# Optimization experiments

Measured on AMD Instinct MI355X. Metric: run time of the kernel, lower is better.

Reference implementation:

```python
import jax, jax.numpy as jnp
import numpy as np
import math

N_HEAD = 16
N_LATENTS = 64
CHUNK = 128
ROPE_THETA = 10000.0


def _rope_cos_sin(T, D, theta):
    # D = head_dim; freqs over D/2 pairs
    inv = 1.0 / (theta ** (jnp.arange(0, D, 2, dtype=jnp.float32) / D))  # [D/2]
    ang = jnp.arange(T, dtype=jnp.float32)[:, None] * inv[None, :]       # [T, D/2]
    return jnp.cos(ang), jnp.sin(ang)


def _apply_rope(k, cos, sin):
    # k: [B, T, H, D]; pairs are consecutive (2i, 2i+1)
    B, T, H, D = k.shape
    kr = k.reshape(B, T, H, D // 2, 2)
    a, b = kr[..., 0], kr[..., 1]
    c = cos[None, :, None, :]
    s = sin[None, :, None, :]
    out = jnp.stack([a * c - b * s, a * s + b * c], axis=-1)
    return out.reshape(B, T, H, D).astype(k.dtype)


def setup_inputs() -> dict:
    key = jax.random.key(0)
    ks = jax.random.split(key, 6)
    B, T, C = 8, 4096, 1024
    H, L = N_HEAD, N_LATENTS
    D = C // H
    std_in = 1.0 / math.sqrt(C)
    return {
        "x": jax.random.normal(ks[0], (B, T, C), jnp.float32),
        "latent_queries": jax.random.normal(ks[1], (1, L, H, D), jnp.float32) * (1.0 / math.sqrt(D)),
        "W_k": jax.random.normal(ks[2], (C, C), jnp.float32) * std_in,
        "W_v": jax.random.normal(ks[3], (C, C), jnp.float32) * std_in,
        "W_g": jax.random.normal(ks[4], (H * L, C), jnp.float32) * std_in,
        "W_p": jax.random.normal(ks[5], (C, C), jnp.float32) * std_in,
    }


def reference(x, latent_queries, W_k, W_v, W_g, W_p):
    B, T, C = x.shape
    H, L, cs = N_HEAD, N_LATENTS, CHUNK
    D = C // H
    scale = 1.0 / math.sqrt(D)

    k = (x @ W_k.T).reshape(B, T, H, D)
    v = (x @ W_v.T).reshape(B, T, H, D)
    cos, sin = _rope_cos_sin(T, D, ROPE_THETA)
    k = _apply_rope(k, cos, sin)

    # softmax-gated latent mixing weights: [B, T, H, L]
    gates = jax.nn.softmax((x @ W_g.T).reshape(B, T, H, L) * scale, axis=-1)

    q = jnp.transpose(latent_queries, (0, 2, 1, 3))          # [1, H, L, D]
    nc = T // cs
    kc = jnp.transpose(k, (0, 2, 1, 3)).reshape(B, H, nc, cs, D)
    vc = jnp.transpose(v, (0, 2, 1, 3)).reshape(B, H, nc, cs, D)

    # per-chunk SDPA with torch is_causal semantics: top-left aligned
    # lower-triangular mask (latent row i attends chunk cols j <= i)
    scores = jnp.einsum('zhld,bhncd->bhnlc', q, kc) * scale   # [B,H,nc,L,cs]
    causal = jnp.arange(cs)[None, :] <= jnp.arange(L)[:, None]  # [L, cs]
    scores = jnp.where(causal[None, None, None], scores, -jnp.inf)
    probs = jax.nn.softmax(scores, axis=-1)
    # matmul with V per chunk, SUM over chunks (as in the torch loop)
    attn = jnp.einsum('bhnlc,bhncd->bhld', probs, vc)         # [B,H,L,D]

    # weighted combine: einsum('bhls,bhtl->bhts') then [B,T,C]
    weighted = jnp.einsum('bhld,bthl->bthd', attn, gates)
    out = weighted.reshape(B, T, C) @ W_p.T
    return out
```

## Files before the change

### kernel.cpp

```cpp
#include <hip/hip_runtime.h>
#include <hip/hip_bf16.h>

typedef unsigned short u16;
typedef __attribute__((ext_vector_type(8))) short bf16x8;
typedef __attribute__((ext_vector_type(4))) float f32x4;
typedef __attribute__((ext_vector_type(4))) unsigned short u16x4;

#define DEVI static __device__ __forceinline__

DEVI u16 f2bf(float f) {
    union { __hip_bfloat16 h; u16 u; } cv;
    cv.h = __float2bfloat16(f);
    return cv.u;
}
DEVI float bf2f(u16 u) {
    union { u16 u; __hip_bfloat16 h; } cv;
    cv.u = u;
    return __bfloat162float(cv.h);
}

DEVI void gload_lds16(const void* g, void* l) {
    __builtin_amdgcn_global_load_lds(
        (const __attribute__((address_space(1))) unsigned int*)g,
        (__attribute__((address_space(3))) unsigned int*)l, 16, 0, 0);
}

__global__ void k_cvt(const float* __restrict__ in, u16* __restrict__ out, int n4) {
    int i = blockIdx.x * blockDim.x + threadIdx.x;
    int stride = gridDim.x * blockDim.x;
    for (; i < n4; i += stride) {
        float4 v = ((const float4*)in)[i];
        u16x4 o;
        o.x = f2bf(v.x); o.y = f2bf(v.y); o.z = f2bf(v.z); o.w = f2bf(v.w);
        ((u16x4*)out)[i] = o;
    }
}

__global__ void k_rope(float2* __restrict__ tab) {
    int i = blockIdx.x * 256 + threadIdx.x;
    int t = i >> 5, j = i & 31;
    float inv = powf(10000.f, -(float)j / 32.f);
    float ang = (float)t * inv;
    float s, c;
    sincosf(ang, &s, &c);
    tab[i] = make_float2(c, s);
}

template<int MODE>
__global__ __launch_bounds__(256, 2) void k_gemm(
    const u16* __restrict__ A, const u16* __restrict__ Bw,
    void* __restrict__ Cout, const float2* __restrict__ rope)
{
    constexpr int K = 1024;
    __shared__ u16 As[128 * 32];
    __shared__ u16 Bs[128 * 32];
    const int tid = threadIdx.x;
    const int lane = tid & 63, wid = tid >> 6;
    const int wr = wid >> 1, wc = wid & 1;
    const int row0 = blockIdx.y * 128, col0 = blockIdx.x * 128;

    int r0 = row0 + (tid >> 2);
    int r1 = r0 + 64;
    if (MODE == 0) {
        r0 = ((r0 >> 11) << 12) | (((r0 >> 6) & 31) << 7) | (r0 & 63);
        r1 = ((r1 >> 11) << 12) | (((r1 >> 6) & 31) << 7) | (r1 & 63);
    }
    const int kcol = (tid & 3) * 8;
    const u16* gA0 = A + (size_t)r0 * K + kcol;
    const u16* gA1 = A + (size_t)r1 * K + kcol;
    const u16* gB0 = Bw + (size_t)(col0 + (tid >> 2)) * K + kcol;
    const u16* gB1 = gB0 + (size_t)64 * K;

    char* AsB = (char*)As + wid * 1024;
    char* BsB = (char*)Bs + wid * 1024;

    f32x4 acc[4][4];
#pragma unroll
    for (int i = 0; i < 4; ++i)
#pragma unroll
        for (int j = 0; j < 4; ++j) acc[i][j] = f32x4{0.f, 0.f, 0.f, 0.f};

#pragma unroll 1
    for (int kt = 0; kt < K / 32; ++kt) {
        gload_lds16(gA0, AsB);
        gload_lds16(gA1, AsB + 4096);
        gload_lds16(gB0, BsB);
        gload_lds16(gB1, BsB + 4096);
        gA0 += 32; gA1 += 32; gB0 += 32; gB1 += 32;
        __syncthreads();
        const int koff = (lane >> 4) * 8;
        bf16x8 af[4], bfr[4];
#pragma unroll
        for (int mf = 0; mf < 4; ++mf)
            af[mf] = *(const bf16x8*)&As[(wr * 64 + mf * 16 + (lane & 15)) * 32 + koff];
#pragma unroll
        for (int nf = 0; nf < 4; ++nf)
            bfr[nf] = *(const bf16x8*)&Bs[(wc * 64 + nf * 16 + (lane & 15)) * 32 + koff];
#pragma unroll
        for (int mf = 0; mf < 4; ++mf)
#pragma unroll
            for (int nf = 0; nf < 4; ++nf)
                acc[mf][nf] = __builtin_amdgcn_mfma_f32_16x16x32_bf16(af[mf], bfr[nf], acc[mf][nf], 0, 0, 0);
        __syncthreads();
    }

    const int rbase = row0 + wr * 64 + (lane >> 4) * 4;
    const int cbase = col0 + wc * 64 + (lane & 15);
#pragma unroll
    for (int mf = 0; mf < 4; ++mf) {
#pragma unroll
        for (int nf = 0; nf < 4; ++nf) {
            const int gc = cbase + nf * 16;
#pragma unroll
            for (int r = 0; r < 4; ++r) {
                const int gr = rbase + mf * 16 + r;
                float v = acc[mf][nf][r];
                if (MODE == 0) {
                    float o = __shfl_xor(v, 1);
                    float res;
                    if (gc < 1024) {
                        int t = (((gr >> 6) & 31) << 7) | (gr & 63);
                        float2 cs = rope[t * 32 + ((gc & 63) >> 1)];
                        res = (gc & 1) ? (o * cs.y + v * cs.x) : (v * cs.x - o * cs.y);
                    } else {
                        res = v;
                    }
                    ((u16*)Cout)[(size_t)gr * 2048 + gc] = f2bf(res);
                } else if (MODE == 1) {
                    ((u16*)Cout)[(size_t)gr * 1024 + gc] = f2bf(v);
                } else {
                    ((float*)Cout)[(size_t)gr * 1024 + gc] = v;
                }
            }
        }
    }
}

__global__ __launch_bounds__(256, 2) void k_attn(
    const u16* __restrict__ kv, const float* __restrict__ lq, float* __restrict__ attnT)
{
    __shared__ char smem[65536];
    const int tid = threadIdx.x;
    const int lane = tid & 63, wid = tid >> 6;
    const int gidx = blockIdx.x & 3;
    const int bh = blockIdx.x >> 2;
    const int b = bh >> 4, h = bh & 15;

    bf16x8 qf[4][2];
#pragma unroll
    for (int lb = 0; lb < 4; ++lb)
#pragma unroll
        for (int kb = 0; kb < 2; ++kb) {
            const float* src = lq + ((size_t)(lb * 16 + (lane & 15)) * 16 + h) * 64 + kb * 32 + (lane >> 4) * 8;
            float4 v0 = ((const float4*)src)[0];
            float4 v1 = ((const float4*)src)[1];
            union { bf16x8 v; u16 u[8]; } pk;
            pk.u[0] = f2bf(v0.x * 0.125f); pk.u[1] = f2bf(v0.y * 0.125f);
            pk.u[2] = f2bf(v0.z * 0.125f); pk.u[3] = f2bf(v0.w * 0.125f);
            pk.u[4] = f2bf(v1.x * 0.125f); pk.u[5] = f2bf(v1.y * 0.125f);
            pk.u[6] = f2bf(v1.z * 0.125f); pk.u[7] = f2bf(v1.w * 0.125f);
            qf[lb][kb] = pk.v;
        }

    char* Pl = smem + wid * 16384;
    char* Vb = smem + wid * 16384 + 8192;
    u16* Vl = (u16*)Vb;

    f32x4 accT[4][4];
#pragma unroll
    for (int i = 0; i < 4; ++i)
#pragma unroll
        for (int j = 0; j < 4; ++j) accT[i][j] = f32x4{0.f, 0.f, 0.f, 0.f};

#pragma unroll 1
    for (int ci = 0; ci < 2; ++ci) {
        const int n = gidx * 8 + wid * 2 + ci;
        const size_t krow = (size_t)b * 2048 + (size_t)n * 64;

#pragma unroll
        for (int j = 0; j < 8; ++j) {
            const u16* g = kv + (krow + j * 8 + (lane >> 3)) * 2048 + 1024 + h * 64 + (lane & 7) * 8;
            gload_lds16(g, Vb + j * 1024);
        }

        f32x4 S[4][4];
#pragma unroll
        for (int i = 0; i < 4; ++i)
#pragma unroll
            for (int j = 0; j < 4; ++j) S[i][j] = f32x4{0.f, 0.f, 0.f, 0.f};
#pragma unroll
        for (int kb = 0; kb < 2; ++kb) {
            bf16x8 kf[4];
#pragma unroll
            for (int cb = 0; cb < 4; ++cb)
                kf[cb] = *(const bf16x8*)(kv + (krow + cb * 16 + (lane & 15)) * 2048 + h * 64 + kb * 32 + (lane >> 4) * 8);
#pragma unroll
            for (int lb = 0; lb < 4; ++lb)
#pragma unroll
                for (int cb = 0; cb < 4; ++cb)
                    S[lb][cb] = __builtin_amdgcn_mfma_f32_16x16x32_bf16(qf[lb][kb], kf[cb], S[lb][cb], 0, 0, 0);
        }

#pragma unroll
        for (int lb = 0; lb < 4; ++lb) {
#pragma unroll
            for (int r = 0; r < 4; ++r) {
                const int l = lb * 16 + (lane >> 4) * 4 + r;
                const int c0 = lane & 15;
                float vv[4];
                float m = -3e30f;
#pragma unroll
                for (int cb = 0; cb < 4; ++cb) {
                    int c = cb * 16 + c0;
                    vv[cb] = (c <= l) ? S[lb][cb][r] : -3e30f;
                    m = fmaxf(m, vv[cb]);
                }
                m = fmaxf(m, __shfl_xor(m, 1));
                m = fmaxf(m, __shfl_xor(m, 2));
                m = fmaxf(m, __shfl_xor(m, 4));
                m = fmaxf(m, __shfl_xor(m, 8));
                float p[4];
                float sum = 0.f;
#pragma unroll
                for (int cb = 0; cb < 4; ++cb) {
                    int c = cb * 16 + c0;
                    p[cb] = (c <= l) ? __expf(vv[cb] - m) : 0.f;
                    sum += p[cb];
                }
                sum += __shfl_xor(sum, 1);
                sum += __shfl_xor(sum, 2);
                sum += __shfl_xor(sum, 4);
                sum += __shfl_xor(sum, 8);
                const float inv = 1.f / sum;
#pragma unroll
                for (int cb = 0; cb < 4; ++cb) {
                    int c = cb * 16 + c0;
                    int byte = (l * 128 + c * 2) ^ ((l & 7) << 4);
                    *(u16*)(Pl + byte) = f2bf(p[cb] * inv);
                }
            }
        }

        asm volatile("s_waitcnt vmcnt(0)" ::: "memory");

#pragma unroll
        for (int kb = 0; kb < 2; ++kb) {
            bf16x8 pf[4];
#pragma unroll
            for (int lf = 0; lf < 4; ++lf) {
                int l = lf * 16 + (lane & 15);
                int byte = (l * 128 + (kb * 32 + (lane >> 4) * 8) * 2) ^ ((l & 7) << 4);
                pf[lf] = *(const bf16x8*)(Pl + byte);
            }
#pragma unroll
            for (int mf = 0; mf < 4; ++mf) {
                const int d = mf * 16 + (lane & 15);
                const int cb2 = kb * 32 + (lane >> 4) * 8;
                union { bf16x8 v; u16 u[8]; } vt;
#pragma unroll
                for (int e = 0; e < 8; ++e) vt.u[e] = Vl[(cb2 + e) * 64 + d];
#pragma unroll
                for (int lf = 0; lf < 4; ++lf)
                    accT[mf][lf] = __builtin_amdgcn_mfma_f32_16x16x32_bf16(vt.v, pf[lf], accT[mf][lf], 0, 0, 0);
            }
        }
    }

    float* red = (float*)smem;
#pragma unroll
    for (int mf = 0; mf < 4; ++mf)
#pragma unroll
        for (int lf = 0; lf < 4; ++lf)
#pragma unroll
            for (int r = 0; r < 4; ++r)
                red[wid * 4096 + (mf * 16 + (lane >> 4) * 4 + r) * 64 + lf * 16 + (lane & 15)] = accT[mf][lf][r];
    __syncthreads();
    for (int idx = tid; idx < 4096; idx += 256) {
        float s = red[idx] + red[4096 + idx] + red[8192 + idx] + red[12288 + idx];
        atomicAdd(&attnT[(size_t)bh * 4096 + idx], s);
    }
}

__global__ __launch_bounds__(256, 4) void k_weighted(
    const u16* __restrict__ logits, const float* __restrict__ attnT, u16* __restrict__ wout)
{
    const int tid = threadIdx.x, lane = tid & 63, wid = tid >> 6;
    const int bh = blockIdx.x >> 5, tt = blockIdx.x & 31;
    const int b = bh >> 4, h = bh & 15;
    const int t0 = tt * 128 + wid * 32;

    const float* at = attnT + (size_t)bh * 4096;
    bf16x8 bfr[4][2];
#pragma unroll
    for (int nf = 0; nf < 4; ++nf)
#pragma unroll
        for (int kb = 0; kb < 2; ++kb) {
            const float* src = at + (nf * 16 + (lane & 15)) * 64 + kb * 32 + (lane >> 4) * 8;
            float4 v0 = ((const float4*)src)[0];
            float4 v1 = ((const float4*)src)[1];
            union { bf16x8 v; u16 u[8]; } pk;
            pk.u[0] = f2bf(v0.x); pk.u[1] = f2bf(v0.y); pk.u[2] = f2bf(v0.z); pk.u[3] = f2bf(v0.w);
            pk.u[4] = f2bf(v1.x); pk.u[5] = f2bf(v1.y); pk.u[6] = f2bf(v1.z); pk.u[7] = f2bf(v1.w);
            bfr[nf][kb] = pk.v;
        }

    f32x4 acc[2][4];
#pragma unroll
    for (int i = 0; i < 2; ++i)
#pragma unroll
        for (int j = 0; j < 4; ++j) acc[i][j] = f32x4{0.f, 0.f, 0.f, 0.f};

#pragma unroll
    for (int mf = 0; mf < 2; ++mf) {
        const int t = t0 + mf * 16 + (lane & 15);
        const u16* lrow = logits + ((size_t)b * 4096 + t) * 1024 + h * 64 + (lane >> 4) * 8;
        bf16x8 l0 = *(const bf16x8*)lrow;
        bf16x8 l1 = *(const bf16x8*)(lrow + 32);
        float va[16];
#pragma unroll
        for (int j = 0; j < 8; ++j) {
            va[j] = bf2f((u16)l0[j]) * 0.125f;
            va[8 + j] = bf2f((u16)l1[j]) * 0.125f;
        }
        float m = va[0];
#pragma unroll
        for (int j = 1; j < 16; ++j) m = fmaxf(m, va[j]);
        m = fmaxf(m, __shfl_xor(m, 16));
        m = fmaxf(m, __shfl_xor(m, 32));
        float sum = 0.f;
#pragma unroll
        for (int j = 0; j < 16; ++j) { va[j] = __expf(va[j] - m); sum += va[j]; }
        sum += __shfl_xor(sum, 16);
        sum += __shfl_xor(sum, 32);
        const float inv = 1.f / sum;
        union { bf16x8 v; u16 u[8]; } a0, a1;
#pragma unroll
        for (int j = 0; j < 8; ++j) {
            a0.u[j] = f2bf(va[j] * inv);
            a1.u[j] = f2bf(va[8 + j] * inv);
        }
#pragma unroll
        for (int nf = 0; nf < 4; ++nf) {
            acc[mf][nf] = __builtin_amdgcn_mfma_f32_16x16x32_bf16(a0.v, bfr[nf][0], acc[mf][nf], 0, 0, 0);
            acc[mf][nf] = __builtin_amdgcn_mfma_f32_16x16x32_bf16(a1.v, bfr[nf][1], acc[mf][nf], 0, 0, 0);
        }
    }

#pragma unroll
    for (int mf = 0; mf < 2; ++mf)
#pragma unroll
        for (int nf = 0; nf < 4; ++nf)
#pragma unroll
            for (int r = 0; r < 4; ++r) {
                int t = t0 + mf * 16 + (lane >> 4) * 4 + r;
                wout[((size_t)b * 4096 + t) * 1024 + h * 64 + nf * 16 + (lane & 15)] = f2bf(acc[mf][nf][r]);
            }
}

extern "C" void kernel_launch(void* const* d_in, const int* in_sizes, int n_in,
                              void* d_out, int out_size, void* d_ws, size_t ws_size,
                              hipStream_t stream)
{
    const float* x  = (const float*)d_in[0];
    const float* lq = (const float*)d_in[1];
    const float* Wk = (const float*)d_in[2];
    const float* Wv = (const float*)d_in[3];
    const float* Wg = (const float*)d_in[4];
    const float* Wp = (const float*)d_in[5];

    char* ws = (char*)d_ws;
    u16*    wkv   = (u16*)(ws + 0);
    u16*    wg    = (u16*)(ws + 4194304);
    u16*    wp    = (u16*)(ws + 6291456);
    float2* rope  = (float2*)(ws + 8388608);
    float*  attnT = (float*)(ws + 9437184);
    u16*    kv    = (u16*)(ws + 11534336);
    u16* logits = (u16*)d_out;
    u16* xb     = (u16*)((char*)d_out + 67108864);

    hipMemsetAsync(attnT, 0, 128 * 4096 * sizeof(float), stream);

    k_cvt<<<2048, 256, 0, stream>>>(x, xb, 33554432 / 4);
    k_cvt<<<512, 256, 0, stream>>>(Wk, wkv, 1048576 / 4);
    k_cvt<<<512, 256, 0, stream>>>(Wv, wkv + 1048576, 1048576 / 4);
    k_cvt<<<512, 256, 0, stream>>>(Wg, wg, 1048576 / 4);
    k_cvt<<<512, 256, 0, stream>>>(Wp, wp, 1048576 / 4);
    k_rope<<<512, 256, 0, stream>>>(rope);

    k_gemm<0><<<dim3(16, 128), 256, 0, stream>>>(xb, wkv, kv, rope);
    k_gemm<1><<<dim3(8, 256), 256, 0, stream>>>(xb, wg, logits, nullptr);
    k_attn<<<512, 256, 0, stream>>>(kv, lq, attnT);
    k_weighted<<<4096, 256, 0, stream>>>(logits, attnT, kv);
    k_gemm<2><<<dim3(8, 256), 256, 0, stream>>>(kv, wp, d_out, nullptr);
}
```

Measured before the change: 613.5 us.

## Replace 128x128 GEMM with pipelined 256x256 tile kernel and XCD-aware block mapping

Rewrites the bf16 GEMM used for the K/V, gate and output projections as a 512-thread, 256x256-tile kernel with a 64-wide K step. It double-buffers 128 KB of dynamic LDS and issues global-to-LDS loads several stages ahead, using explicit vmcnt waits and barriers. It also raises MFMA priority with s_setprio and remaps block indices so neighbouring tiles land on the same XCD. The aim is to hide memory latency and raise operand reuse per LDS load. In exchange it uses far more LDS and registers per block, and the hand-placed waitcnt and barrier schedule is fragile.

```diff
diff --git a/kernel.cpp b/kernel.cpp
--- a/kernel.cpp
+++ b/kernel.cpp
@@ -24,6 +24,9 @@
         (const __attribute__((address_space(1))) unsigned int*)g,
         (__attribute__((address_space(3))) unsigned int*)l, 16, 0, 0);
 }
+
+#define BAR asm volatile("s_barrier" ::: "memory")
+#define VMW(N) asm volatile("s_waitcnt vmcnt(" #N ")" ::: "memory")
 
 __global__ void k_cvt(const float* __restrict__ in, u16* __restrict__ out, int n4) {
     int i = blockIdx.x * blockDim.x + threadIdx.x;
@@ -47,67 +50,116 @@
 }
 
 template<int MODE>
-__global__ __launch_bounds__(256, 2) void k_gemm(
+__global__ __launch_bounds__(512, 2) void k_gemm256(
     const u16* __restrict__ A, const u16* __restrict__ Bw,
     void* __restrict__ Cout, const float2* __restrict__ rope)
 {
-    constexpr int K = 1024;
-    __shared__ u16 As[128 * 32];
-    __shared__ u16 Bs[128 * 32];
+    extern __shared__ char lds[];
     const int tid = threadIdx.x;
     const int lane = tid & 63, wid = tid >> 6;
-    const int wr = wid >> 1, wc = wid & 1;
-    const int row0 = blockIdx.y * 128, col0 = blockIdx.x * 128;
-
-    int r0 = row0 + (tid >> 2);
-    int r1 = r0 + 64;
-    if (MODE == 0) {
-        r0 = ((r0 >> 11) << 12) | (((r0 >> 6) & 31) << 7) | (r0 & 63);
-        r1 = ((r1 >> 11) << 12) | (((r1 >> 6) & 31) << 7) | (r1 & 63);
-    }
-    const int kcol = (tid & 3) * 8;
-    const u16* gA0 = A + (size_t)r0 * K + kcol;
-    const u16* gA1 = A + (size_t)r1 * K + kcol;
-    const u16* gB0 = Bw + (size_t)(col0 + (tid >> 2)) * K + kcol;
-    const u16* gB1 = gB0 + (size_t)64 * K;
-
-    char* AsB = (char*)As + wid * 1024;
-    char* BsB = (char*)Bs + wid * 1024;
-
-    f32x4 acc[4][4];
-#pragma unroll
-    for (int i = 0; i < 4; ++i)
-#pragma unroll
-        for (int j = 0; j < 4; ++j) acc[i][j] = f32x4{0.f, 0.f, 0.f, 0.f};
+    const int wr = wid >> 2, wc = wid & 3;
+    const int koff = (lane >> 4) * 16;
+
+    const int GX = (MODE == 0) ? 8 : 4;
+    const int kx = GX >> 1;
+    int orig = blockIdx.x + blockIdx.y * GX;
+    int xcd = orig & 7, i = orig >> 3;
+    int bx = (xcd % kx) * 2 + (i & 1);
+    int by = (xcd / kx) * 32 + (i >> 1);
+    const int row0 = by * 256, col0 = bx * 256;
+
+    auto stage = [&](int s) {
+        const int t = s >> 2;
+        const int isB = s & 1;
+        const int kh = (s >> 1) & 1;
+        char* base = lds + isB * 65536 + (t & 1) * 32768 + kh * 16384;
+        const int kbase = t * 64 + kh * 32;
+#pragma unroll
+        for (int j = 0; j < 2; ++j) {
+            int idx = j * 512 + tid;
+            int r = idx >> 2;
+            int kc = idx & 3;
+            int grow;
+            if (isB) {
+                grow = col0 + r;
+            } else {
+                grow = row0 + r;
+                if (MODE == 0)
+                    grow = ((grow >> 11) << 12) | (((grow >> 6) & 31) << 7) | (grow & 63);
+            }
+            const u16* g = (isB ? Bw : A) + (size_t)grow * 1024 + kbase + kc * 8;
+            gload_lds16(g, base + j * 8192 + wid * 1024);
+        }
+    };
+
+    bf16x8 af[8];
+    bf16x8 bq[2];
+    f32x4 acc[8][4];
+#pragma unroll
+    for (int m = 0; m < 8; ++m)
+#pragma unroll
+        for (int n = 0; n < 4; ++n) acc[m][n] = f32x4{0.f, 0.f, 0.f, 0.f};
+
+#define LDA(T, KH) do { \
+    const char* ab_ = lds + ((T) & 1) * 32768 + (KH) * 16384; \
+    _Pragma("unroll") \
+    for (int mf = 0; mf < 8; ++mf) \
+        af[mf] = *(const bf16x8*)(ab_ + (wr * 128 + mf * 16 + (lane & 15)) * 64 + koff); \
+} while (0)
+
+#define LDB(T, KH, NH) do { \
+    const char* bb_ = lds + 65536 + ((T) & 1) * 32768 + (KH) * 16384; \
+    bq[0] = *(const bf16x8*)(bb_ + (wc * 64 + ((NH) * 2)     * 16 + (lane & 15)) * 64 + koff); \
+    bq[1] = *(const bf16x8*)(bb_ + (wc * 64 + ((NH) * 2 + 1) * 16 + (lane & 15)) * 64 + koff); \
+} while (0)
+
+#define MMA(NH) do { \
+    __builtin_amdgcn_s_setprio(1); \
+    _Pragma("unroll") \
+    for (int mf = 0; mf < 8; ++mf) { \
+        acc[mf][2 * (NH)]     = __builtin_amdgcn_mfma_f32_16x16x32_bf16(af[mf], bq[0], acc[mf][2 * (NH)], 0, 0, 0); \
+        acc[mf][2 * (NH) + 1] = __builtin_amdgcn_mfma_f32_16x16x32_bf16(af[mf], bq[1], acc[mf][2 * (NH) + 1], 0, 0, 0); \
+    } \
+    __builtin_amdgcn_s_setprio(0); \
+} while (0)
 
 #pragma unroll 1
-    for (int kt = 0; kt < K / 32; ++kt) {
-        gload_lds16(gA0, AsB);
-        gload_lds16(gA1, AsB + 4096);
-        gload_lds16(gB0, BsB);
-        gload_lds16(gB1, BsB + 4096);
-        gA0 += 32; gA1 += 32; gB0 += 32; gB1 += 32;
-        __syncthreads();
-        const int koff = (lane >> 4) * 8;
-        bf16x8 af[4], bfr[4];
-#pragma unroll
-        for (int mf = 0; mf < 4; ++mf)
-            af[mf] = *(const bf16x8*)&As[(wr * 64 + mf * 16 + (lane & 15)) * 32 + koff];
-#pragma unroll
-        for (int nf = 0; nf < 4; ++nf)
-            bfr[nf] = *(const bf16x8*)&Bs[(wc * 64 + nf * 16 + (lane & 15)) * 32 + koff];
-#pragma unroll
-        for (int mf = 0; mf < 4; ++mf)
-#pragma unroll
-            for (int nf = 0; nf < 4; ++nf)
-                acc[mf][nf] = __builtin_amdgcn_mfma_f32_16x16x32_bf16(af[mf], bfr[nf], acc[mf][nf], 0, 0, 0);
-        __syncthreads();
-    }
-
-    const int rbase = row0 + wr * 64 + (lane >> 4) * 4;
+    for (int s = 0; s < 7; ++s) stage(s);
+    VMW(10);
+    BAR;
+
+#pragma unroll 1
+    for (int t = 0; t < 14; ++t) {
+        LDA(t, 0); LDB(t, 0, 0);
+        stage(4 * t + 7);
+        BAR; MMA(0); BAR;
+        LDB(t, 0, 1);
+        stage(4 * t + 8);
+        BAR; MMA(1); VMW(10); BAR;
+        LDA(t, 1); LDB(t, 1, 0);
+        stage(4 * t + 9);
+        BAR; MMA(0); BAR;
+        LDB(t, 1, 1);
+        stage(4 * t + 10);
+        BAR; MMA(1); VMW(10); BAR;
+    }
+    LDA(14, 0); LDB(14, 0, 0); stage(63); BAR; MMA(0); BAR;
+    LDB(14, 0, 1);                         BAR; MMA(1); VMW(8); BAR;
+    LDA(14, 1); LDB(14, 1, 0);             BAR; MMA(0); BAR;
+    LDB(14, 1, 1);                         BAR; MMA(1); VMW(4); BAR;
+    LDA(15, 0); LDB(15, 0, 0);             BAR; MMA(0); BAR;
+    LDB(15, 0, 1);                         BAR; MMA(1); VMW(0); BAR;
+    LDA(15, 1); LDB(15, 1, 0);             BAR; MMA(0); BAR;
+    LDB(15, 1, 1);                         BAR; MMA(1);
+
+#undef LDA
+#undef LDB
+#undef MMA
+
+    const int rbase = row0 + wr * 128 + ((lane >> 4) << 2);
     const int cbase = col0 + wc * 64 + (lane & 15);
 #pragma unroll
-    for (int mf = 0; mf < 4; ++mf) {
+    for (int mf = 0; mf < 8; ++mf) {
 #pragma unroll
         for (int nf = 0; nf < 4; ++nf) {
             const int gc = cbase + nf * 16;
@@ -378,6 +430,10 @@
     u16* logits = (u16*)d_out;
     u16* xb     = (u16*)((char*)d_out + 67108864);
 
+    hipFuncSetAttribute((const void*)k_gemm256<0>, hipFuncAttributeMaxDynamicSharedMemorySize, 131072);
+    hipFuncSetAttribute((const void*)k_gemm256<1>, hipFuncAttributeMaxDynamicSharedMemorySize, 131072);
+    hipFuncSetAttribute((const void*)k_gemm256<2>, hipFuncAttributeMaxDynamicSharedMemorySize, 131072);
+
     hipMemsetAsync(attnT, 0, 128 * 4096 * sizeof(float), stream);
 
     k_cvt<<<2048, 256, 0, stream>>>(x, xb, 33554432 / 4);
@@ -387,9 +443,9 @@
     k_cvt<<<512, 256, 0, stream>>>(Wp, wp, 1048576 / 4);
     k_rope<<<512, 256, 0, stream>>>(rope);
 
-    k_gemm<0><<<dim3(16, 128), 256, 0, stream>>>(xb, wkv, kv, rope);
-    k_gemm<1><<<dim3(8, 256), 256, 0, stream>>>(xb, wg, logits, nullptr);
+    k_gemm256<0><<<dim3(8, 64), 512, 131072, stream>>>(xb, wkv, kv, rope);
+    k_gemm256<1><<<dim3(4, 128), 512, 131072, stream>>>(xb, wg, logits, nullptr);
     k_attn<<<512, 256, 0, stream>>>(kv, lq, attnT);
     k_weighted<<<4096, 256, 0, stream>>>(logits, attnT, kv);
-    k_gemm<2><<<dim3(8, 256), 256, 0, stream>>>(kv, wp, d_out, nullptr);
-}
+    k_gemm256<2><<<dim3(4, 128), 512, 131072, stream>>>(kv, wp, d_out, nullptr);
+}
```

Measured after the change: 581.3 us. -5.2%, faster.
